# Optimization experiments

Measured on AMD Instinct MI355X. Metric: run time of the kernel, lower is better.

Reference implementation:

```python
import jax, jax.numpy as jnp
import numpy as np

NEG_BIG = -9e15


def gat_layer(h, adj, W, a, alpha, concat):
    # h: (N, Fin), W: (Fin, Fout), a: (2*Fout, 1)
    Wh = h @ W                                   # (N, Fout)
    F = Wh.shape[1]
    # e[i,j] = LeakyReLU(cat(Wh_i, Wh_j) @ a) = LeakyReLU(s_i + d_j)
    s = Wh @ a[:F, 0]                            # (N,)
    d = Wh @ a[F:, 0]                            # (N,)
    e = jax.nn.leaky_relu(s[:, None] + d[None, :], negative_slope=alpha)  # (N, N)
    e = jnp.where(adj > 0, e, NEG_BIG)
    att = jax.nn.softmax(e, axis=1)              # (N, N)
    out = att @ Wh                               # (N, Fout)
    return jax.nn.elu(out) if concat else out


def setup_inputs() -> dict:
    key = jax.random.key(0)
    ks = jax.random.split(key, 12)
    N, nfeat, nhid, nlatent, nclass = 8192, 512, 256, 64, 16

    def xavier(k, shape):
        gain = 1.414
        fan_in, fan_out = shape[0], shape[1]
        bound = gain * np.sqrt(6.0 / (fan_in + fan_out))
        return jax.random.uniform(k, shape, jnp.float32, -bound, bound)

    x = jax.random.normal(ks[0], (N, nfeat), jnp.float32)
    adj = jax.random.randint(ks[1], (N, N), 0, 2, jnp.int32)
    eps = jax.random.normal(ks[2], (N, nlatent), jnp.float32)
    return {
        "x": x,
        "adj": adj,
        "eps": eps,
        "W1": xavier(ks[3], (nfeat, nhid)),
        "a1": xavier(ks[4], (2 * nhid, 1)),
        "Wmu": xavier(ks[5], (nhid, nlatent)),
        "amu": xavier(ks[6], (2 * nlatent, 1)),
        "Wlv": xavier(ks[7], (nhid, nlatent)),
        "alv": xavier(ks[8], (2 * nlatent, 1)),
        "Wc": xavier(ks[9], (nlatent, nclass)),
        "bc": jnp.zeros((nclass,), jnp.float32),
    }


def reference(x, adj, eps, W1, a1, Wmu, amu, Wlv, alv, Wc, bc):
    alpha = 0.2  # LeakyReLU negative slope
    # eval mode: all dropouts are identity
    h = gat_layer(x, adj, W1, a1, alpha, concat=True)      # (N, nhid)
    mu = gat_layer(h, adj, Wmu, amu, alpha, concat=False)  # (N, nlatent)
    logvar = gat_layer(h, adj, Wlv, alv, alpha, concat=False)
    z = mu + eps * jnp.exp(0.5 * logvar)
    logits = z @ Wc + bc                                   # (N, nclass)
    return logits, mu, logvar
```

## Files before the change

### kernel.cpp

```cpp
#include <hip/hip_runtime.h>

typedef unsigned short u16;
typedef __attribute__((ext_vector_type(8))) short short8;
typedef __attribute__((ext_vector_type(4))) float f32x4;

#define NROW 8192

__device__ __forceinline__ float bf2f(u16 h) {
  unsigned u = ((unsigned)h) << 16;
  return __builtin_bit_cast(float, u);
}
__device__ __forceinline__ float ldf(const void* p, size_t i, int f32) {
  return f32 ? ((const float*)p)[i] : bf2f(((const u16*)p)[i]);
}
__device__ __forceinline__ u16 f2bf(float f) {
  unsigned b = __builtin_bit_cast(unsigned, f);
  b += 0x7FFFu + ((b >> 16) & 1u);
  return (u16)(b >> 16);
}

__global__ void detect3(const u16* __restrict__ xr, unsigned* __restrict__ mode) {
  __shared__ int zc, bg;
  int t = threadIdx.x;
  if (t == 0) { zc = 0; bg = 0; }
  __syncthreads();
  int zeros_even = 0; int big = 0;
  for (int i = t; i < 4096; i += 256) {
    u16 v = xr[i];
    if (!(i & 1) && v == 0) zeros_even++;
    if (fabsf(bf2f(v)) > 1e6f) big = 1;
  }
  atomicAdd(&zc, zeros_even);
  if (big) atomicOr(&bg, 1);
  __syncthreads();
  if (t == 0) *mode = (zc > 512 || bg) ? 1u : 0u;
}

__global__ void detect_adj(const unsigned* __restrict__ a, unsigned* __restrict__ amode) {
  __shared__ int clo;
  int t = threadIdx.x;
  if (t == 0) clo = 0;
  __syncthreads();
  int c = 0;
  for (int i = t; i < 4096; i += 256)
    if (a[i] == 0x00003F80u) c++;
  atomicAdd(&clo, c);
  __syncthreads();
  if (t == 0) *amode = (clo > 32) ? 1u : 0u;
}

struct AdjRaw { int4 w0, w1; };
__device__ __forceinline__ AdjRaw adj_load(const void* adj, size_t base, int amode) {
  AdjRaw r;
  if (amode == 0) {
    const int4* p = (const int4*)((const int*)adj + base);
    r.w0 = p[0]; r.w1 = p[1];
  } else {
    r.w0 = *(const int4*)((const u16*)adj + base);
    r.w1 = make_int4(0, 0, 0, 0);
  }
  return r;
}
__device__ __forceinline__ void adj_decode(const AdjRaw& r, int amode, int* aa) {
  if (amode == 0) {
    aa[0] = r.w0.x != 0; aa[1] = r.w0.y != 0; aa[2] = r.w0.z != 0; aa[3] = r.w0.w != 0;
    aa[4] = r.w1.x != 0; aa[5] = r.w1.y != 0; aa[6] = r.w1.z != 0; aa[7] = r.w1.w != 0;
  } else {
    aa[0] = (r.w0.x & 0xFFFF) != 0; aa[1] = ((unsigned)r.w0.x >> 16) != 0;
    aa[2] = (r.w0.y & 0xFFFF) != 0; aa[3] = ((unsigned)r.w0.y >> 16) != 0;
    aa[4] = (r.w0.z & 0xFFFF) != 0; aa[5] = ((unsigned)r.w0.z >> 16) != 0;
    aa[6] = (r.w0.w & 0xFFFF) != 0; aa[7] = ((unsigned)r.w0.w >> 16) != 0;
  }
}

__global__ __launch_bounds__(256) void gemm_mfma(const u16* __restrict__ Abf,
    const u16* __restrict__ BT, float* __restrict__ C, int K, int N) {
  int tid = threadIdx.x;
  int l = tid & 63, w = tid >> 6;
  int m0 = blockIdx.y * 64, n0 = blockIdx.x * 64;
  const u16* arow = Abf + (size_t)(m0 + w * 16 + (l & 15)) * K + (l >> 4) * 8;
  const u16* brow = BT + (size_t)(n0 + (l & 15)) * K + (l >> 4) * 8;
  f32x4 acc[4];
#pragma unroll
  for (int nt = 0; nt < 4; ++nt) acc[nt] = (f32x4){0.f, 0.f, 0.f, 0.f};
  for (int k0 = 0; k0 < K; k0 += 32) {
    short8 a = *(const short8*)(arow + k0);
#pragma unroll
    for (int nt = 0; nt < 4; ++nt) {
      short8 b = *(const short8*)(brow + (size_t)nt * 16 * K + k0);
      acc[nt] = __builtin_amdgcn_mfma_f32_16x16x32_bf16(a, b, acc[nt], 0, 0, 0);
    }
  }
#pragma unroll
  for (int nt = 0; nt < 4; ++nt)
#pragma unroll
    for (int q = 0; q < 4; ++q)
      C[(size_t)(m0 + w * 16 + (l >> 4) * 4 + q) * N + n0 + nt * 16 + (l & 15)] =
          acc[nt][q];
}

__global__ __launch_bounds__(256) void gemm2_dual(const u16* __restrict__ Abf,
    const u16* __restrict__ BT0, const u16* __restrict__ BT1,
    float* __restrict__ C0, float* __restrict__ C1) {
  const int K = 256, N = 64;
  const u16* BT = blockIdx.x ? BT1 : BT0;
  float* C = blockIdx.x ? C1 : C0;
  int tid = threadIdx.x, l = tid & 63, w = tid >> 6;
  int m0 = blockIdx.y * 64;
  const u16* arow = Abf + (size_t)(m0 + w * 16 + (l & 15)) * K + (l >> 4) * 8;
  const u16* brow = BT + (size_t)(l & 15) * K + (l >> 4) * 8;
  f32x4 acc[4];
#pragma unroll
  for (int nt = 0; nt < 4; ++nt) acc[nt] = (f32x4){0.f, 0.f, 0.f, 0.f};
  for (int k0 = 0; k0 < K; k0 += 32) {
    short8 a = *(const short8*)(arow + k0);
#pragma unroll
    for (int nt = 0; nt < 4; ++nt) {
      short8 b = *(const short8*)(brow + (size_t)nt * 16 * K + k0);
      acc[nt] = __builtin_amdgcn_mfma_f32_16x16x32_bf16(a, b, acc[nt], 0, 0, 0);
    }
  }
#pragma unroll
  for (int nt = 0; nt < 4; ++nt)
#pragma unroll
    for (int q = 0; q < 4; ++q)
      C[(size_t)(m0 + w * 16 + (l >> 4) * 4 + q) * N + nt * 16 + (l & 15)] = acc[nt][q];
}

__global__ __launch_bounds__(256) void convert_bf16(const void* __restrict__ in,
    u16* __restrict__ out, int n8, const unsigned* __restrict__ modep) {
  int f32 = (int)*modep;
  int i = blockIdx.x * 256 + threadIdx.x;
  if (i >= n8) return;
  if (f32) {
    float4 v0 = ((const float4*)in)[(size_t)i * 2];
    float4 v1 = ((const float4*)in)[(size_t)i * 2 + 1];
    ushort4 o0 = {f2bf(v0.x), f2bf(v0.y), f2bf(v0.z), f2bf(v0.w)};
    ushort4 o1 = {f2bf(v1.x), f2bf(v1.y), f2bf(v1.z), f2bf(v1.w)};
    ((ushort4*)out)[(size_t)i * 2] = o0;
    ((ushort4*)out)[(size_t)i * 2 + 1] = o1;
  } else {
    ((int4*)out)[i] = ((const int4*)in)[i];
  }
}

__global__ __launch_bounds__(256) void transpose_bf16(const float* __restrict__ in,
    u16* __restrict__ out, int M, int F) {
  __shared__ float t[32][33];
  int m0 = blockIdx.x * 32, f0 = blockIdx.y * 32;
  int c = threadIdx.x & 31, r = threadIdx.x >> 5;
  for (int rr = r; rr < 32; rr += 8)
    t[rr][c] = in[(size_t)(m0 + rr) * F + f0 + c];
  __syncthreads();
  for (int rr = r; rr < 32; rr += 8)
    out[(size_t)(f0 + rr) * M + m0 + c] = f2bf(t[c][rr]);
}

__global__ __launch_bounds__(256) void transpose_pair(const float* __restrict__ in0,
    const float* __restrict__ in1, u16* __restrict__ out0, u16* __restrict__ out1,
    int M, int F) {
  const float* in = blockIdx.z ? in1 : in0;
  u16* out = blockIdx.z ? out1 : out0;
  __shared__ float t[32][33];
  int m0 = blockIdx.x * 32, f0 = blockIdx.y * 32;
  int c = threadIdx.x & 31, r = threadIdx.x >> 5;
  for (int rr = r; rr < 32; rr += 8)
    t[rr][c] = in[(size_t)(m0 + rr) * F + f0 + c];
  __syncthreads();
  for (int rr = r; rr < 32; rr += 8)
    out[(size_t)(f0 + rr) * M + m0 + c] = f2bf(t[c][rr]);
}

__global__ __launch_bounds__(256) void transpose_any(const void* __restrict__ in,
    u16* __restrict__ out, int M, int F, const unsigned* __restrict__ modep) {
  int f32 = (int)*modep;
  __shared__ u16 t[32][33];
  int m0 = blockIdx.x * 32, f0 = blockIdx.y * 32;
  int c = threadIdx.x & 31, r = threadIdx.x >> 5;
  for (int rr = r; rr < 32; rr += 8)
    t[rr][c] = f2bf(ldf(in, (size_t)(m0 + rr) * F + f0 + c, f32));
  __syncthreads();
  for (int rr = r; rr < 32; rr += 8)
    out[(size_t)(f0 + rr) * M + m0 + c] = t[c][rr];
}

__global__ __launch_bounds__(256) void transpose_w2(const void* __restrict__ in0,
    const void* __restrict__ in1, u16* __restrict__ out0, u16* __restrict__ out1,
    int M, int F, const unsigned* __restrict__ modep) {
  int f32 = (int)*modep;
  const void* in = blockIdx.z ? in1 : in0;
  u16* out = blockIdx.z ? out1 : out0;
  __shared__ u16 t[32][33];
  int m0 = blockIdx.x * 32, f0 = blockIdx.y * 32;
  int c = threadIdx.x & 31, r = threadIdx.x >> 5;
  for (int rr = r; rr < 32; rr += 8)
    t[rr][c] = f2bf(ldf(in, (size_t)(m0 + rr) * F + f0 + c, f32));
  __syncthreads();
  for (int rr = r; rr < 32; rr += 8)
    out[(size_t)(f0 + rr) * M + m0 + c] = t[c][rr];
}

__global__ __launch_bounds__(256) void sd_f32(const float* __restrict__ Wh,
    const void* __restrict__ a2, float* __restrict__ s, float* __restrict__ d,
    int F, const unsigned* __restrict__ modep) {
  int f32 = (int)*modep;
  int row = blockIdx.x * 4 + (threadIdx.x >> 6);
  int l = threadIdx.x & 63;
  float ss = 0.f, dd = 0.f;
  for (int k = l; k < F; k += 64) {
    float wv = Wh[(size_t)row * F + k];
    ss += wv * ldf(a2, k, f32);
    dd += wv * ldf(a2, F + k, f32);
  }
#pragma unroll
  for (int off = 32; off > 0; off >>= 1) {
    ss += __shfl_down(ss, off, 64);
    dd += __shfl_down(dd, off, 64);
  }
  if (l == 0) { s[row] = ss; d[row] = dd; }
}

__global__ __launch_bounds__(256) void sd_dual(const float* __restrict__ Wh0,
    const float* __restrict__ Wh1, const void* __restrict__ a0,
    const void* __restrict__ a1, float* __restrict__ s0, float* __restrict__ s1,
    float* __restrict__ d0, float* __restrict__ d1,
    const unsigned* __restrict__ modep) {
  int f32 = (int)*modep;
  int L = blockIdx.y;
  const float* Wh = L ? Wh1 : Wh0;
  const void* a2 = L ? a1 : a0;
  int row = blockIdx.x * 4 + (threadIdx.x >> 6);
  int l = threadIdx.x & 63;
  float wv = Wh[(size_t)row * 64 + l];
  float ss = wv * ldf(a2, l, f32);
  float dd = wv * ldf(a2, 64 + l, f32);
#pragma unroll
  for (int off = 32; off > 0; off >>= 1) {
    ss += __shfl_down(ss, off, 64);
    dd += __shfl_down(dd, off, 64);
  }
  if (l == 0) { (L ? s1 : s0)[row] = ss; (L ? d1 : d0)[row] = dd; }
}

__global__ __launch_bounds__(256) void dmax_reduce(const float* __restrict__ da,
    const float* __restrict__ db, float* __restrict__ cells) {
  const float* d = blockIdx.x ? db : da;
  __shared__ float red[256];
  float m = -3.4e38f;
  for (int i = threadIdx.x; i < NROW; i += 256) m = fmaxf(m, d[i]);
  red[threadIdx.x] = m;
  __syncthreads();
#pragma unroll
  for (int sft = 128; sft > 0; sft >>= 1) {
    if (threadIdx.x < sft) red[threadIdx.x] = fmaxf(red[threadIdx.x], red[threadIdx.x + sft]);
    __syncthreads();
  }
  if (threadIdx.x == 0) cells[blockIdx.x * 16] = red[0];
}

__device__ __forceinline__ int pa_off(int L, int s, int mh, int row, int kg) {
  return ((L * 4 + s * 2 + mh) << 10) + (row << 6) + ((kg ^ ((row >> 1) & 3)) << 4);
}

template <int NL, int FDIM, int JS>
__global__ __launch_bounds__(256) void flash_mfma(
    const u16* __restrict__ whTa, const u16* __restrict__ whTb,
    const float* __restrict__ sa, const float* __restrict__ da,
    const float* __restrict__ sb, const float* __restrict__ db,
    const float* __restrict__ cella, const float* __restrict__ cellb,
    const void* __restrict__ adj, const unsigned* __restrict__ amodep,
    float* __restrict__ acca, float* __restrict__ lsa,
    float* __restrict__ accb, float* __restrict__ lsb) {
  constexpr int JLEN = NROW / JS;
  constexpr int NIT = JLEN / 64;
  constexpr int NTW = (NL == 1) ? 4 : 2;
  constexpr int NRBLK = NROW / 32;
  __shared__ __align__(16) char PA[2][NL * 4096];
  __shared__ float ddl[2][NL][64];
  __shared__ float sv_[NL][32], Ms_[NL][32];
  int tid = threadIdx.x;
  int amode = (int)*amodep;
  int rblk = blockIdx.x % NRBLK, js = blockIdx.x / NRBLK;
  int r0 = rblk * 32;
  size_t jbase = (size_t)js * JLEN;
  if (tid < 32 * NL) {
    int L = tid >> 5, i = tid & 31;
    float Dm = L ? *cellb : *cella;
    float t0 = (L ? sb : sa)[r0 + i];
    sv_[L][i] = t0;
    float m = t0 + Dm;
    Ms_[L][i] = fmaxf(m, 0.2f * m);
  }
  if (tid < 64 * NL) {
    int L = tid >> 6, i = tid & 63;
    ddl[0][L][i] = (L ? db : da)[jbase + i];
  }
  __syncthreads();
  int sr = tid >> 3, sjo = tid & 7;
  int s_w = sjo >> 2, kg_w = sjo & 3, mh_w = sr >> 4, row_w = sr & 15;
  int l = tid & 63, w = tid >> 6;
  int layer = (NL == 1) ? 0 : (w >> 1);
  int ntb = (NL == 1) ? (w * 4) : ((w & 1) * 2);
  const u16* whT = layer ? whTb : whTa;
  f32x4 acc[2][NTW];
#pragma unroll
  for (int m = 0; m < 2; ++m)
#pragma unroll
    for (int n = 0; n < NTW; ++n) acc[m][n] = (f32x4){0.f, 0.f, 0.f, 0.f};
  float psum[NL];
#pragma unroll
  for (int L = 0; L < NL; ++L) psum[L] = 0.f;
  size_t abase = (size_t)(r0 + sr) * NROW + jbase + sjo * 8;

  AdjRaw araw = adj_load(adj, abase, amode);
  for (int it = 0; it < NIT; ++it) {
    size_t j0 = jbase + (size_t)it * 64;
    int cur = it & 1;
    if (it + 1 < NIT && tid < 64 * NL) {
      int L = tid >> 6, i = tid & 63;
      ddl[cur ^ 1][L][i] = (L ? db : da)[j0 + 64 + i];
    }
    short8 bfr[2][NTW];
#pragma unroll
    for (int s2 = 0; s2 < 2; ++s2) {
      size_t jcol = j0 + s2 * 32 + (size_t)(l >> 4) * 8;
#pragma unroll
      for (int nt = 0; nt < NTW; ++nt)
        bfr[s2][nt] =
            *(const short8*)&whT[(size_t)((ntb + nt) * 16 + (l & 15)) * NROW + jcol];
    }
    AdjRaw anext = araw;
    if (it + 1 < NIT) anext = adj_load(adj, abase + (size_t)(it + 1) * 64, amode);
    int aa[8];
    adj_decode(araw, amode, aa);
    char* pab = PA[cur];
#pragma unroll
    for (int L = 0; L < NL; ++L) {
      float sv = sv_[L][sr], Mr = Ms_[L][sr];
      short8 pk;
      float ps = 0.f;
#pragma unroll
      for (int q = 0; q < 8; ++q) {
        float t = sv + ddl[cur][L][sjo * 8 + q];
        float e = fmaxf(t, 0.2f * t) - Mr;
        float p = aa[q] ? __expf(e) : 0.f;
        ps += p;
        pk[q] = (short)f2bf(p);
      }
      psum[L] += ps;
      *(short8*)(pab + pa_off(L, s_w, mh_w, row_w, kg_w)) = pk;
    }
    __syncthreads();
    __builtin_amdgcn_s_setprio(1);
#pragma unroll
    for (int s2 = 0; s2 < 2; ++s2) {
      short8 a0 = *(const short8*)(pab + pa_off(layer, s2, 0, l & 15, l >> 4));
      short8 a1 = *(const short8*)(pab + pa_off(layer, s2, 1, l & 15, l >> 4));
#pragma unroll
      for (int nt = 0; nt < NTW; ++nt) {
        acc[0][nt] = __builtin_amdgcn_mfma_f32_16x16x32_bf16(a0, bfr[s2][nt],
                                                             acc[0][nt], 0, 0, 0);
        acc[1][nt] = __builtin_amdgcn_mfma_f32_16x16x32_bf16(a1, bfr[s2][nt],
                                                             acc[1][nt], 0, 0, 0);
      }
    }
    __builtin_amdgcn_s_setprio(0);
    araw = anext;
  }
  __syncthreads();
  float* red = (float*)PA;
#pragma unroll
  for (int L = 0; L < NL; ++L) red[L * 256 + sr * 8 + sjo] = psum[L];
  __syncthreads();
  if (tid < 32 * NL) {
    int L = tid >> 5, r = tid & 31;
    float t = 0.f;
#pragma unroll
    for (int q = 0; q < 8; ++q) t += red[L * 256 + r * 8 + q];
    atomicAdd(&(L ? lsb : lsa)[r0 + r], t);
  }
  float* accp = layer ? accb : acca;
#pragma unroll
  for (int m = 0; m < 2; ++m)
#pragma unroll
    for (int nt = 0; nt < NTW; ++nt)
#pragma unroll
      for (int q = 0; q < 4; ++q)
        atomicAdd(&accp[(size_t)(r0 + m * 16 + (l >> 4) * 4 + q) * FDIM +
                        (ntb + nt) * 16 + (l & 15)],
                  acc[m][nt][q]);
}

__global__ __launch_bounds__(256) void combine_elu(const float* __restrict__ acc_g,
    const float* __restrict__ lsum_g, u16* __restrict__ hbf) {
  int idx = blockIdx.x * 256 + threadIdx.x;
  float x = acc_g[idx] / lsum_g[idx >> 8];
  x = (x > 0.f) ? x : (__expf(x) - 1.f);
  hbf[idx] = f2bf(x);
}

__global__ __launch_bounds__(256) void combine_div(const float* __restrict__ acc_g,
    const float* __restrict__ lsum_g, float* __restrict__ outf, float* __restrict__ outd) {
  int idx = blockIdx.x * 256 + threadIdx.x;
  float x = acc_g[idx] / lsum_g[idx >> 6];
  outf[idx] = x;
  outd[idx] = x;
}

__global__ __launch_bounds__(256) void logits_f32(const float* __restrict__ mu,
    const float* __restrict__ lv, const void* __restrict__ eps,
    const void* __restrict__ Wc, const void* __restrict__ bcv,
    float* __restrict__ outL, const unsigned* __restrict__ modep) {
  int f32 = (int)*modep;
  __shared__ float zs[64 * 64];
  __shared__ float wcs[64 * 16];
  int tid = threadIdx.x;
  for (int i = tid; i < 1024; i += 256) wcs[i] = ldf(Wc, i, f32);
  int rl = tid >> 2, cs = (tid & 3) * 16;
  int row = blockIdx.x * 64 + rl;
  size_t rb64 = (size_t)row * 64;
  for (int c = cs; c < cs + 16; ++c)
    zs[rl * 64 + c] = mu[rb64 + c] + ldf(eps, rb64 + c, f32) * __expf(0.5f * lv[rb64 + c]);
  __syncthreads();
  for (int it = tid; it < 1024; it += 256) {
    int r = it >> 4, oc = it & 15;
    float a = ldf(bcv, oc, f32);
    for (int c = 0; c < 64; ++c) a += zs[r * 64 + c] * wcs[c * 16 + oc];
    outL[(size_t)(blockIdx.x * 64 + r) * 16 + oc] = a;
  }
}

extern "C" void kernel_launch(void* const* d_in, const int* in_sizes, int n_in,
                              void* d_out, int out_size, void* d_ws, size_t ws_size,
                              hipStream_t stream) {
  (void)out_size; (void)ws_size;
  int ix = 0, iadj = 1, ieps = 2, iW1 = 3, ia1 = 4, iWmu = 5, iamu = 6,
      iWlv = 7, ialv = 8, iWc = 9, ibc = 10;
  {
    int fmu = -1, flv = -1, fam = -1, fal = -1;
    for (int i = 0; i < n_in; ++i) {
      switch (in_sizes[i]) {
        case 67108864: iadj = i; break;
        case 4194304:  ix   = i; break;
        case 524288:   ieps = i; break;
        case 131072:   iW1  = i; break;
        case 512:      ia1  = i; break;
        case 1024:     iWc  = i; break;
        case 16:       ibc  = i; break;
        case 16384:    if (fmu < 0) fmu = i; else flv = i; break;
        case 128:      if (fam < 0) fam = i; else fal = i; break;
        default: break;
      }
    }
    if (fmu >= 0 && flv >= 0) { iWmu = fmu; iWlv = flv; }
    if (fam >= 0 && fal >= 0) { iamu = fam; ialv = fal; }
  }
  const void* adj = d_in[iadj];
  char* ws = (char*)d_ws;
  const size_t KB = 1024, MB = 1024 * 1024;
  float* wh1   = (float*)(ws + 0);
  float* whmu  = (float*)(ws + 0);
  float* whlv  = (float*)(ws + 2 * MB);
  float* muf   = (float*)(ws + 4 * MB);
  float* lvf   = (float*)(ws + 6 * MB);
  u16*   xbf   = (u16*)(ws + 8 * MB);
  u16*   whT1  = (u16*)(ws + 8 * MB);
  u16*   hbf   = (u16*)(ws + 12 * MB);
  float* hacc  = (float*)(ws + 16 * MB);
  float* macc  = (float*)(ws + 16 * MB);
  float* lvacc = (float*)(ws + 18 * MB);
  u16*   whmuT = (u16*)(ws + 20 * MB);
  u16*   whlvT = (u16*)(ws + 21 * MB);
  u16*   W1T   = (u16*)(ws + 22 * MB);
  u16*   WmuT  = (u16*)(ws + 22 * MB + 256 * KB);
  u16*   WlvT  = (u16*)(ws + 22 * MB + 288 * KB);
  float* lsum1 = (float*)(ws + 24 * MB);
  float* lsmu  = (float*)(ws + 24 * MB + 32 * KB);
  float* lslv  = (float*)(ws + 24 * MB + 64 * KB);
  float* s1    = (float*)(ws + 24 * MB + 96 * KB);
  float* d1    = (float*)(ws + 24 * MB + 128 * KB);
  float* smu   = (float*)(ws + 24 * MB + 160 * KB);
  float* dmu   = (float*)(ws + 24 * MB + 192 * KB);
  float* slv   = (float*)(ws + 24 * MB + 224 * KB);
  float* dlv   = (float*)(ws + 24 * MB + 256 * KB);
  float* dmaxv = (float*)(ws + 24 * MB + 288 * KB);
  unsigned* mode  = (unsigned*)(ws + 24 * MB + 289 * KB);
  unsigned* amode = (unsigned*)(ws + 24 * MB + 290 * KB);

  float* out_logits = (float*)d_out;
  float* out_mu     = (float*)d_out + 131072;
  float* out_lv     = (float*)d_out + 655360;

  (void)hipMemsetAsync(lsum1, 0, 96 * KB, stream);
  (void)hipMemsetAsync(hacc, 0, 8 * MB, stream);
  detect3<<<1, 256, 0, stream>>>((const u16*)d_in[ix], mode);
  detect_adj<<<1, 256, 0, stream>>>((const unsigned*)adj, amode);

  convert_bf16<<<2048, 256, 0, stream>>>(d_in[ix], xbf, 524288, mode);
  transpose_any<<<dim3(16, 8), 256, 0, stream>>>(d_in[iW1], W1T, 512, 256, mode);
  gemm_mfma<<<dim3(4, 128), 256, 0, stream>>>(xbf, W1T, wh1, 512, 256);
  transpose_bf16<<<dim3(256, 8), 256, 0, stream>>>(wh1, whT1, 8192, 256);
  sd_f32<<<2048, 256, 0, stream>>>(wh1, d_in[ia1], s1, d1, 256, mode);
  dmax_reduce<<<1, 256, 0, stream>>>(d1, d1, dmaxv + 0);
  flash_mfma<1, 256, 8><<<2048, 256, 0, stream>>>(whT1, nullptr, s1, d1,
      nullptr, nullptr, dmaxv + 0, nullptr, adj, amode, hacc, lsum1, nullptr, nullptr);
  combine_elu<<<8192, 256, 0, stream>>>(hacc, lsum1, hbf);

  (void)hipMemsetAsync(macc, 0, 4 * MB, stream);

  transpose_w2<<<dim3(8, 2, 2), 256, 0, stream>>>(d_in[iWmu], d_in[iWlv],
      WmuT, WlvT, 256, 64, mode);
  gemm2_dual<<<dim3(2, 128), 256, 0, stream>>>(hbf, WmuT, WlvT, whmu, whlv);
  transpose_pair<<<dim3(256, 2, 2), 256, 0, stream>>>(whmu, whlv, whmuT, whlvT,
      8192, 64);
  sd_dual<<<dim3(2048, 2), 256, 0, stream>>>(whmu, whlv, d_in[iamu], d_in[ialv],
      smu, slv, dmu, dlv, mode);
  dmax_reduce<<<2, 256, 0, stream>>>(dmu, dlv, dmaxv + 16);
  flash_mfma<2, 64, 8><<<2048, 256, 0, stream>>>(whmuT, whlvT, smu, dmu, slv, dlv,
      dmaxv + 16, dmaxv + 32, adj, amode, macc, lsmu, lvacc, lslv);
  combine_div<<<2048, 256, 0, stream>>>(macc, lsmu, muf, out_mu);
  combine_div<<<2048, 256, 0, stream>>>(lvacc, lslv, lvf, out_lv);

  logits_f32<<<128, 256, 0, stream>>>(muf, lvf, d_in[ieps], d_in[iWc], d_in[ibc], out_logits, mode);
}
```

Measured before the change: 690.1 us.

## Preload d-vector slice to LDS, deepen adjacency prefetch, use lighter barrier

Loads the block's whole slice of the destination-score vector into shared memory once, as float4, instead of double-buffering 64 floats per iteration. Each thread then reads its 8 values as two float4 LDS loads. The adjacency prefetch is deepened from one to two iterations ahead to hide more global-memory latency. The per-iteration __syncthreads is replaced by an explicit lgkmcnt wait, a raw s_barrier and a sched_barrier so outstanding global loads are not waited on. This costs more LDS and registers, which may reduce occupancy.

```diff
diff --git a/kernel.cpp b/kernel.cpp
--- a/kernel.cpp
+++ b/kernel.cpp
@@ -276,7 +276,7 @@
   constexpr int NTW = (NL == 1) ? 4 : 2;
   constexpr int NRBLK = NROW / 32;
   __shared__ __align__(16) char PA[2][NL * 4096];
-  __shared__ float ddl[2][NL][64];
+  __shared__ __align__(16) float dd_[NL][JLEN];
   __shared__ float sv_[NL][32], Ms_[NL][32];
   int tid = threadIdx.x;
   int amode = (int)*amodep;
@@ -291,9 +291,9 @@
     float m = t0 + Dm;
     Ms_[L][i] = fmaxf(m, 0.2f * m);
   }
-  if (tid < 64 * NL) {
-    int L = tid >> 6, i = tid & 63;
-    ddl[0][L][i] = (L ? db : da)[jbase + i];
+  for (int u = tid; u < (NL * JLEN) / 4; u += 256) {
+    int L = u / (JLEN / 4), uu = u - L * (JLEN / 4);
+    ((float4*)dd_[L])[uu] = ((const float4*)((L ? db : da) + jbase))[uu];
   }
   __syncthreads();
   int sr = tid >> 3, sjo = tid & 7;
@@ -312,14 +312,11 @@
   for (int L = 0; L < NL; ++L) psum[L] = 0.f;
   size_t abase = (size_t)(r0 + sr) * NROW + jbase + sjo * 8;
 
-  AdjRaw araw = adj_load(adj, abase, amode);
+  AdjRaw adjA = adj_load(adj, abase, amode);
+  AdjRaw adjB = (NIT > 1) ? adj_load(adj, abase + 64, amode) : adjA;
   for (int it = 0; it < NIT; ++it) {
     size_t j0 = jbase + (size_t)it * 64;
     int cur = it & 1;
-    if (it + 1 < NIT && tid < 64 * NL) {
-      int L = tid >> 6, i = tid & 63;
-      ddl[cur ^ 1][L][i] = (L ? db : da)[j0 + 64 + i];
-    }
     short8 bfr[2][NTW];
 #pragma unroll
     for (int s2 = 0; s2 < 2; ++s2) {
@@ -329,19 +326,22 @@
         bfr[s2][nt] =
             *(const short8*)&whT[(size_t)((ntb + nt) * 16 + (l & 15)) * NROW + jcol];
     }
-    AdjRaw anext = araw;
-    if (it + 1 < NIT) anext = adj_load(adj, abase + (size_t)(it + 1) * 64, amode);
+    AdjRaw adjN = adjB;
+    if (it + 2 < NIT) adjN = adj_load(adj, abase + (size_t)(it + 2) * 64, amode);
     int aa[8];
-    adj_decode(araw, amode, aa);
+    adj_decode(adjA, amode, aa);
     char* pab = PA[cur];
 #pragma unroll
     for (int L = 0; L < NL; ++L) {
       float sv = sv_[L][sr], Mr = Ms_[L][sr];
+      float4 dv0 = *(const float4*)&dd_[L][it * 64 + sjo * 8];
+      float4 dv1 = *(const float4*)&dd_[L][it * 64 + sjo * 8 + 4];
+      float dvv[8] = {dv0.x, dv0.y, dv0.z, dv0.w, dv1.x, dv1.y, dv1.z, dv1.w};
       short8 pk;
       float ps = 0.f;
 #pragma unroll
       for (int q = 0; q < 8; ++q) {
-        float t = sv + ddl[cur][L][sjo * 8 + q];
+        float t = sv + dvv[q];
         float e = fmaxf(t, 0.2f * t) - Mr;
         float p = aa[q] ? __expf(e) : 0.f;
         ps += p;
@@ -350,7 +350,9 @@
       psum[L] += ps;
       *(short8*)(pab + pa_off(L, s_w, mh_w, row_w, kg_w)) = pk;
     }
-    __syncthreads();
+    asm volatile("s_waitcnt lgkmcnt(0)" ::: "memory");
+    __builtin_amdgcn_s_barrier();
+    __builtin_amdgcn_sched_barrier(0);
     __builtin_amdgcn_s_setprio(1);
 #pragma unroll
     for (int s2 = 0; s2 < 2; ++s2) {
@@ -365,7 +367,7 @@
       }
     }
     __builtin_amdgcn_s_setprio(0);
-    araw = anext;
+    adjA = adjB; adjB = adjN;
   }
   __syncthreads();
   float* red = (float*)PA;
```

New measurement: 673.9 us. 1.02x faster.
